# Optimization experiments

Hardware: AMD Instinct MI355X
Metric: run time of the kernel (lower is better)

Reference implementation:

```python
import jax, jax.numpy as jnp
import numpy as np

B, T, C, H = 8, 1024, 1024, 16
HD = C // H  # head dim = 64
NEG = -1e9


def setup_inputs() -> dict:
    key = jax.random.key(0)
    ks = jax.random.split(key, 10)
    total = B * T
    x = jax.random.normal(ks[0], (total, C), dtype=jnp.float32)
    # identity pack: each padded row is a contiguous chunk of tokens
    padpack_index = jnp.arange(total, dtype=jnp.int64).reshape(B, T)
    # sorted per-row sequence ids -> block-diagonal attention within each packed row
    padpack_batch = jnp.sort(jax.random.randint(ks[1], (B, T), 0, 4, dtype=jnp.int32), axis=-1)
    padpack_inverse_index = jnp.arange(total, dtype=jnp.int64)
    s = 1.0 / np.sqrt(C)
    Wq = jax.random.uniform(ks[2], (C, C), jnp.float32, -s, s)
    bq = jax.random.uniform(ks[3], (C,), jnp.float32, -s, s)
    Wk = jax.random.uniform(ks[4], (C, C), jnp.float32, -s, s)
    bk = jax.random.uniform(ks[5], (C,), jnp.float32, -s, s)
    Wv = jax.random.uniform(ks[6], (C, C), jnp.float32, -s, s)
    bv = jax.random.uniform(ks[7], (C,), jnp.float32, -s, s)
    Wp = jax.random.uniform(ks[8], (C, C), jnp.float32, -s, s)
    bp = jax.random.uniform(ks[9], (C,), jnp.float32, -s, s)
    return {"x": x, "padpack_index": padpack_index, "padpack_batch": padpack_batch,
            "padpack_inverse_index": padpack_inverse_index,
            "Wq": Wq, "bq": bq, "Wk": Wk, "bk": bk, "Wv": Wv, "bv": bv, "Wp": Wp, "bp": bp}


def reference(x, padpack_index, padpack_batch, padpack_inverse_index,
              Wq, bq, Wk, bk, Wv, bv, Wp, bp):
    # gather ragged tokens into padded [B, T, C]
    xp = x[padpack_index]
    # torch Linear: y = x @ W.T + b
    q = (xp @ Wq.T + bq).reshape(B, T, H, HD)
    k = (xp @ Wk.T + bk).reshape(B, T, H, HD)
    v = (xp @ Wv.T + bv).reshape(B, T, H, HD)
    scale = 1.0 / np.sqrt(HD).astype(np.float32)
    att = jnp.einsum('bihd,bjhd->bhij', q, k) * scale  # [B,H,T,T]
    # mask: token pairs from different packed sequences cannot attend
    mask = (padpack_batch[:, :, None] != padpack_batch[:, None, :])[:, None]  # [B,1,T,T]
    att = jnp.where(mask, NEG, att)
    att = jax.nn.softmax(att, axis=-1)
    y = jnp.einsum('bhij,bjhd->bihd', att, v).reshape(B, T, C)
    y = y @ Wp.T + bp
    # scatter back to ragged layout [total_tokens, C]
    return y.reshape(B * T, C)[padpack_inverse_index]
```

## Files before the change

### kernel.cpp

```cpp
#include <hip/hip_runtime.h>


typedef __attribute__((ext_vector_type(8))) short short8;
typedef __attribute__((ext_vector_type(4))) float f32x4;

#define MFMA16(a, b, c) __builtin_amdgcn_mfma_f32_16x16x32_bf16((a), (b), (c), 0, 0, 0)

__device__ __forceinline__ ushort f2b(float f) {
  union { float f; unsigned u; } v; v.f = f;
  unsigned u = v.u;
  return (ushort)((u + 0x7fffu + ((u >> 16) & 1u)) >> 16);
}

__device__ __forceinline__ void gload16(const void* g, void* l) {
  __builtin_amdgcn_global_load_lds((const __attribute__((address_space(1))) unsigned int*)g,
                                   (__attribute__((address_space(3))) unsigned int*)l,
                                   16, 0, 0);
}

__device__ __forceinline__ void cvt4(const float* __restrict__ s, ushort* __restrict__ d) {
  const float4 v = *(const float4*)s;
  ushort4 r; r.x = f2b(v.x); r.y = f2b(v.y); r.z = f2b(v.z); r.w = f2b(v.w);
  *(ushort4*)d = r;
}

__global__ __launch_bounds__(256) void prep(const float* __restrict__ x,
    const float* __restrict__ wq, const float* __restrict__ wk,
    const float* __restrict__ wv, const float* __restrict__ wp,
    ushort* __restrict__ xb, ushort* __restrict__ wb) {
  const long long e0 = ((long long)blockIdx.x * 256 + threadIdx.x) * 4;
  const long long NX = 8388608ll;
  if (e0 < NX) {
    cvt4(x + e0, xb + e0);
  } else {
    const long long t = e0 - NX;
    const int sel = (int)(t >> 20);
    const float* w = sel == 0 ? wq : sel == 1 ? wk : sel == 2 ? wv : wp;
    cvt4(w + (t & 1048575), wb + t);
  }
}

__global__ void seg_bounds(const int* __restrict__ pb, int* __restrict__ bnd) {
  const int b = blockIdx.x, i = threadIdx.x;
  const int* p = pb + b * 1024;
  const int cur = p[i];
  const int prev = (i == 0) ? -1 : p[i - 1];
  for (int v = prev + 1; v <= cur; ++v) bnd[b * 8 + v] = i;
  if (i == 1023)
    for (int v = cur + 1; v <= 4; ++v) bnd[b * 8 + v] = 1024;
}

template <int BN, int WM, int WN, int MODE>
__global__ __launch_bounds__(512, 2) void gemm8(
    const ushort* __restrict__ A, const ushort* __restrict__ Bw,
    const float* __restrict__ bias0, const float* __restrict__ bias1,
    const float* __restrict__ bias2,
    ushort* __restrict__ O0, ushort* __restrict__ O1, ushort* __restrict__ O2,
    float* __restrict__ Of) {
  constexpr int BM = 256;
  constexpr int MREP = BM / (WM * 16);
  constexpr int NREP = BN / (WN * 16);
  constexpr int ACH = BM * 64;
  constexpr int BCH = BN * 64;
  constexpr int GLA = ACH / 8192;
  constexpr int GLB = BCH / 8192;
  constexpr int GL = GLA + GLB;
  constexpr int BUFB = 2 * (ACH + BCH);
  __shared__ __align__(16) char smem[2 * BUFB];

  const int tid = threadIdx.x, lane = tid & 63, wid = tid >> 6;
  const int wr = wid / WN, wc = wid % WN;
  const int lg = lane >> 4, lc = lane & 15;

  const int id = blockIdx.x;
  const int s = id >> 3;
  const int m0 = ((id & 7) * 4 + (s & 3)) << 8;
  const int n0 = (s >> 2) * BN;

  f32x4 acc[MREP][NREP] = {};

  const int sr0 = tid >> 2;
  const int sc0 = (tid & 3) ^ ((sr0 >> 1) & 3);

#define STAGE_PAIR(p, kh, kt) { \
    char* ad = smem + (p) * BUFB + (kh) * ACH; \
    char* bd = smem + (p) * BUFB + 2 * ACH + (kh) * BCH; \
    const int kcol = (kt) * 64 + (kh) * 32; \
    gload16(A + (size_t)(m0 + sr0) * 1024 + kcol + sc0 * 8, ad + tid * 16); \
    if constexpr (GLA == 2) \
      gload16(A + (size_t)(m0 + 128 + sr0) * 1024 + kcol + sc0 * 8, ad + (tid + 512) * 16); \
    gload16(Bw + (size_t)(n0 + sr0) * 1024 + kcol + sc0 * 8, bd + tid * 16); \
    if constexpr (GLB == 2) \
      gload16(Bw + (size_t)(n0 + 128 + sr0) * 1024 + kcol + sc0 * 8, bd + (tid + 512) * 16); \
  }

#define PHASE_COMPUTE(p, kh) { \
    const char* ab = smem + (p) * BUFB + (kh) * ACH; \
    const char* bb = smem + (p) * BUFB + 2 * ACH + (kh) * BCH; \
    short8 af[MREP]; short8 bf[NREP]; \
    _Pragma("unroll") \
    for (int f = 0; f < MREP; ++f) { \
      const int row = wr * (MREP * 16) + f * 16 + lc; \
      af[f] = *(const short8*)(ab + row * 64 + ((lg ^ ((row >> 1) & 3)) << 4)); \
    } \
    _Pragma("unroll") \
    for (int g = 0; g < NREP; ++g) { \
      const int row = wc * (NREP * 16) + g * 16 + lc; \
      bf[g] = *(const short8*)(bb + row * 64 + ((lg ^ ((row >> 1) & 3)) << 4)); \
    } \
    asm volatile("s_waitcnt lgkmcnt(0)" ::: "memory"); \
    __builtin_amdgcn_sched_barrier(0); \
    __builtin_amdgcn_s_setprio(1); \
    _Pragma("unroll") \
    for (int f = 0; f < MREP; ++f) \
      _Pragma("unroll") \
      for (int g = 0; g < NREP; ++g) \
        acc[f][g] = MFMA16(af[f], bf[g], acc[f][g]); \
    __builtin_amdgcn_s_setprio(0); \
  }

#define WAIT_VM_GL() { \
    if constexpr (GL == 4) asm volatile("s_waitcnt vmcnt(4)" ::: "memory"); \
    else asm volatile("s_waitcnt vmcnt(3)" ::: "memory"); }

  STAGE_PAIR(0, 0, 0)
  STAGE_PAIR(0, 1, 0)

#pragma unroll 2
  for (int i = 0; i < 30; ++i) {
    const int t = i >> 1, kh = i & 1, p = t & 1;
    WAIT_VM_GL()
    __builtin_amdgcn_s_barrier();
    __builtin_amdgcn_sched_barrier(0);
    STAGE_PAIR(p ^ 1, kh, t + 1)
    PHASE_COMPUTE(p, kh)
  }
  WAIT_VM_GL()
  __builtin_amdgcn_s_barrier();
  __builtin_amdgcn_sched_barrier(0);
  PHASE_COMPUTE(1, 0)
  asm volatile("s_waitcnt vmcnt(0)" ::: "memory");
  __builtin_amdgcn_s_barrier();
  __builtin_amdgcn_sched_barrier(0);
  PHASE_COMPUTE(1, 1)

  if constexpr (MODE == 0) {
    const int sel = n0 >> 10, nloc = n0 & 1023;
    const float* bias = sel == 0 ? bias0 : sel == 1 ? bias1 : bias2;
    float bval[NREP];
#pragma unroll
    for (int g = 0; g < NREP; ++g) bval[g] = bias[nloc + wc * (NREP * 16) + g * 16 + lc];
    if (sel < 2) {
      ushort* dst = sel ? O1 : O0;
#pragma unroll
      for (int f = 0; f < MREP; ++f)
#pragma unroll
        for (int j = 0; j < 4; ++j) {
          const size_t row = m0 + wr * (MREP * 16) + f * 16 + lg * 4 + j;
#pragma unroll
          for (int g = 0; g < NREP; ++g)
            dst[row * 1024 + nloc + wc * (NREP * 16) + g * 16 + lc] =
                f2b(acc[f][g][j] + bval[g]);
        }
    } else {
      ushort (*Ts)[264] = (ushort(*)[264])smem;
#pragma unroll
      for (int mh = 0; mh < 2; ++mh) {
        __syncthreads();
        if (wr == mh) {
#pragma unroll
          for (int f = 0; f < MREP; ++f)
#pragma unroll
            for (int g = 0; g < NREP; ++g)
#pragma unroll
              for (int j = 0; j < 4; ++j)
                Ts[f * 16 + lg * 4 + j][wc * (NREP * 16) + g * 16 + lc] =
                    f2b(acc[f][g][j] + bval[g]);
        }
        __syncthreads();
        const int c = tid >> 1, th = (tid & 1) * 64;
        const int gt = m0 + mh * 128;
        const int b = gt >> 10, t0 = (gt & 1023) + th;
        const int gc = nloc + c;
        ushort* dp = O2 + ((size_t)((b * 16 + (gc >> 6)) * 64 + (gc & 63))) * 1024 + t0;
#pragma unroll
        for (int gb = 0; gb < 8; ++gb) {
          short8 pk;
#pragma unroll
          for (int u = 0; u < 8; ++u) pk[u] = (short)Ts[th + gb * 8 + u][c];
          *(short8*)(dp + gb * 8) = pk;
        }
      }
    }
  } else {
    float bval[NREP];
#pragma unroll
    for (int g = 0; g < NREP; ++g) bval[g] = bias0[n0 + wc * (NREP * 16) + g * 16 + lc];
#pragma unroll
    for (int f = 0; f < MREP; ++f)
#pragma unroll
      for (int j = 0; j < 4; ++j) {
        const size_t row = m0 + wr * (MREP * 16) + f * 16 + lg * 4 + j;
#pragma unroll
        for (int g = 0; g < NREP; ++g)
          Of[row * 1024 + n0 + wc * (NREP * 16) + g * 16 + lc] = acc[f][g][j] + bval[g];
      }
  }
#undef STAGE_PAIR
#undef PHASE_COMPUTE
#undef WAIT_VM_GL
}

__global__ __launch_bounds__(256) void attn(const ushort* __restrict__ Q,
    const ushort* __restrict__ K, const ushort* __restrict__ Vt,
    const int* __restrict__ bnd, ushort* __restrict__ O) {
  __shared__ __align__(16) char kvbuf[2][16384];
  __shared__ __align__(16) ushort Plds[4][16][68];

  const int tid = threadIdx.x, lane = tid & 63, w = tid >> 6;
  const int lg = lane >> 4, lc = lane & 15;

  const int id = blockIdx.x;
  const int xcd = id & 7, slot = id >> 3;
  const int bh = xcd + 8 * (slot >> 4), qt = slot & 15;
  const int b = bh >> 4, h = bh & 15;
  const int q0 = qt * 64 + w * 16;

  const int* bd = bnd + b * 8;
  const int b1 = bd[1], b2 = bd[2], b3 = bd[3], b4 = bd[4];
#define SEGID(k) (((k) >= b1) + ((k) >= b2) + ((k) >= b3) + ((k) >= b4))

  const int qid = SEGID(q0 + lc);
  int klo_l = (qid > 0) ? b1 : 0;
  klo_l = (qid > 1) ? b2 : klo_l;
  klo_l = (qid > 2) ? b3 : klo_l;
  int khi_l = (qid > 0) ? b2 : b1;
  khi_l = (qid > 1) ? b3 : khi_l;
  khi_l = (qid > 2) ? b4 : khi_l;

  const int bq_lo = SEGID(qt * 64), bq_hi = SEGID(qt * 64 + 63);
  unsigned am = 0;
#pragma unroll
  for (int jt = 0; jt < 16; ++jt) {
    const int tlo = SEGID(jt * 64), thi = SEGID(jt * 64 + 63);
    if (thi >= bq_lo && tlo <= bq_hi) am |= (1u << jt);
  }

  const ushort* qp = Q + (size_t)(b * 1024 + q0 + lc) * 1024 + h * 64 + lg * 8;
  const short8 qf0 = *(const short8*)qp;
  const short8 qf1 = *(const short8*)(qp + 32);

  const int r0 = tid >> 3;
  const int c16 = (tid & 7) ^ (r0 & 7);
  const ushort* Kg0 = K + (size_t)(b * 1024 + r0) * 1024 + h * 64 + c16 * 8;
  const ushort* Kg1 = Kg0 + (size_t)32 * 1024;
  const ushort* Vg0 = Vt + (size_t)(bh * 64 + r0) * 1024 + c16 * 8;
  const ushort* Vg1 = Vg0 + (size_t)32 * 1024;

#define STAGE(bufp, j) { \
    gload16(Kg0 + (size_t)(j) * 1024, (bufp) + tid * 16); \
    gload16(Kg1 + (size_t)(j) * 1024, (bufp) + 4096 + tid * 16); \
    gload16(Vg0 + (j), (bufp) + 8192 + tid * 16); \
    gload16(Vg1 + (j), (bufp) + 12288 + tid * 16); }

#define SOFF(r, ch) ((r) * 128 + ((((ch) ^ ((r) & 7))) << 4))

  float mr = -1e30f, lr = 0.f;
  f32x4 o[4] = {};

  unsigned rem = am;
  int jc = __builtin_ctz(rem) * 64;
  rem &= rem - 1;
  STAGE(kvbuf[0], jc)
  __syncthreads();
  int cur = 0;

  for (;;) {
    int jn = -1;
    if (rem) {
      jn = __builtin_ctz(rem) * 64;
      rem &= rem - 1;
      STAGE(kvbuf[cur ^ 1], jn)
    }
    const char* bufK = kvbuf[cur];
    const char* bufV = kvbuf[cur] + 8192;

    short8 kf[8];
#pragma unroll
    for (int n = 0; n < 4; ++n) {
      const int rr = n * 16 + lc;
      kf[2 * n] = *(const short8*)(bufK + SOFF(rr, lg));
      kf[2 * n + 1] = *(const short8*)(bufK + SOFF(rr, lg + 4));
    }
    f32x4 s[4];
    __builtin_amdgcn_s_setprio(1);
#pragma unroll
    for (int n = 0; n < 4; ++n) {
      f32x4 z = {};
      z = MFMA16(kf[2 * n], qf0, z);
      s[n] = MFMA16(kf[2 * n + 1], qf1, z);
    }
    __builtin_amdgcn_s_setprio(0);

#pragma unroll
    for (int n = 0; n < 4; ++n) {
      const int kk = jc + n * 16 + lg * 4;
#pragma unroll
      for (int r = 0; r < 4; ++r) {
        const bool ok = (kk + r >= klo_l) && (kk + r < khi_l);
        s[n][r] = ok ? s[n][r] * 0.125f : -1e9f;
      }
    }

    float rm = fmaxf(fmaxf(fmaxf(s[0][0], s[0][1]), fmaxf(s[0][2], s[0][3])),
                     fmaxf(fmaxf(fmaxf(s[1][0], s[1][1]), fmaxf(s[1][2], s[1][3])),
                           fmaxf(fmaxf(fmaxf(s[2][0], s[2][1]), fmaxf(s[2][2], s[2][3])),
                                 fmaxf(fmaxf(s[3][0], s[3][1]), fmaxf(s[3][2], s[3][3])))));
    rm = fmaxf(rm, __shfl_xor(rm, 16));
    rm = fmaxf(rm, __shfl_xor(rm, 32));
    float mn = mr;
    if (!__all(rm <= mr + 8.f)) {
      mn = fmaxf(mr, rm);
      const float sf = __expf(mr - mn);
      mr = mn;
      lr *= sf;
      const float s0 = __shfl(sf, lg * 4 + 0);
      const float s1 = __shfl(sf, lg * 4 + 1);
      const float s2 = __shfl(sf, lg * 4 + 2);
      const float s3 = __shfl(sf, lg * 4 + 3);
#pragma unroll
      for (int n = 0; n < 4; ++n) {
        o[n][0] *= s0; o[n][1] *= s1; o[n][2] *= s2; o[n][3] *= s3;
      }
    }
    float rs = 0.f;
#pragma unroll
    for (int n = 0; n < 4; ++n)
#pragma unroll
      for (int r = 0; r < 4; ++r) {
        const float p = __expf(s[n][r] - mn);
        s[n][r] = p; rs += p;
      }
    rs += __shfl_xor(rs, 16);
    rs += __shfl_xor(rs, 32);
    lr += rs;

#pragma unroll
    for (int n = 0; n < 4; ++n) {
      ushort4 pk;
      pk.x = f2b(s[n][0]); pk.y = f2b(s[n][1]); pk.z = f2b(s[n][2]); pk.w = f2b(s[n][3]);
      *(ushort4*)&Plds[w][lc][n * 16 + lg * 4] = pk;
    }
    asm volatile("s_waitcnt lgkmcnt(0)" ::: "memory");
    __builtin_amdgcn_sched_barrier(0);
    const short8 p0 = *(const short8*)&Plds[w][lc][lg * 8];
    const short8 p1 = *(const short8*)&Plds[w][lc][32 + lg * 8];
    __builtin_amdgcn_sched_barrier(0);

    short8 vv[8];
#pragma unroll
    for (int n = 0; n < 4; ++n) {
      const int rr = n * 16 + lc;
      vv[2 * n] = *(const short8*)(bufV + SOFF(rr, lg));
      vv[2 * n + 1] = *(const short8*)(bufV + SOFF(rr, lg + 4));
    }
    __builtin_amdgcn_s_setprio(1);
#pragma unroll
    for (int n = 0; n < 4; ++n) {
      o[n] = MFMA16(p0, vv[2 * n], o[n]);
      o[n] = MFMA16(p1, vv[2 * n + 1], o[n]);
    }
    __builtin_amdgcn_s_setprio(0);

    if (jn < 0) break;
    __syncthreads();
    cur ^= 1;
    jc = jn;
  }

  const float linv = 1.f / lr;
  const float i0 = __shfl(linv, lg * 4 + 0);
  const float i1 = __shfl(linv, lg * 4 + 1);
  const float i2 = __shfl(linv, lg * 4 + 2);
  const float i3 = __shfl(linv, lg * 4 + 3);
#pragma unroll
  for (int n = 0; n < 4; ++n) {
    const size_t base = (size_t)(b * 1024 + q0) * 1024 + h * 64 + n * 16 + lc;
    O[base + 0 * 1024 + (size_t)lg * 4096] = f2b(o[n][0] * i0);
    O[base + 1 * 1024 + (size_t)lg * 4096] = f2b(o[n][1] * i1);
    O[base + 2 * 1024 + (size_t)lg * 4096] = f2b(o[n][2] * i2);
    O[base + 3 * 1024 + (size_t)lg * 4096] = f2b(o[n][3] * i3);
  }
#undef STAGE
#undef SOFF
#undef SEGID
}

extern "C" void kernel_launch(void* const* d_in, const int* in_sizes, int n_in,
                              void* d_out, int out_size, void* d_ws, size_t ws_size,
                              hipStream_t stream) {
  const float* x  = (const float*)d_in[0];
  const int*  pb  = (const int*)d_in[2];
  const float* Wq = (const float*)d_in[4]; const float* bq = (const float*)d_in[5];
  const float* Wk = (const float*)d_in[6]; const float* bk = (const float*)d_in[7];
  const float* Wv = (const float*)d_in[8]; const float* bv = (const float*)d_in[9];
  const float* Wp = (const float*)d_in[10]; const float* bp = (const float*)d_in[11];
  float* out = (float*)d_out;
  char* ws = (char*)d_ws;

  ushort* xb = (ushort*)ws;
  ushort* wb = (ushort*)(ws + (16u << 20));
  ushort* Qb = (ushort*)(ws + (24u << 20));
  ushort* Kb = (ushort*)(ws + (40u << 20));
  ushort* Vt = (ushort*)(ws + (56u << 20));
  int*    bnd = (int*)(ws + (72u << 20));
  ushort* Ob = xb;

  prep<<<12288, 256, 0, stream>>>(x, Wq, Wk, Wv, Wp, xb, wb);
  seg_bounds<<<8, 1024, 0, stream>>>(pb, bnd);
  gemm8<256, 2, 4, 0><<<384, 512, 0, stream>>>(xb, wb, bq, bk, bv, Qb, Kb, Vt, nullptr);
  attn<<<2048, 256, 0, stream>>>(Qb, Kb, Vt, bnd, Ob);
  gemm8<128, 4, 2, 1><<<256, 512, 0, stream>>>(Ob, wb + (3 << 20), bp,
                                               nullptr, nullptr, nullptr, nullptr, nullptr, out);
}
```

Measured before the change: 156.1 us.

## Triple-buffer GEMM staging and shrink QKV tile to 256x128

The GEMM kernel now uses three LDS buffers, so loads for k-tile t+2 are issued while tile t is computed, replacing the previous double buffering with deeper prefetch. The QKV projection drops from 256x256 tiles to 256x128 tiles, doubling its grid to 768 blocks for better CU fill; both GEMMs now share one fixed tile shape. The cost is more LDS per block (144KB), which may restrict occupancy to one block per CU despite launch_bounds(512,2), plus more redundant A-tile loads in the QKV GEMM.

```diff
diff --git a/kernel.cpp b/kernel.cpp
--- a/kernel.cpp
+++ b/kernel.cpp
@@ -50,141 +50,149 @@
     for (int v = cur + 1; v <= 4; ++v) bnd[b * 8 + v] = 1024;
 }
 
-template <int BN, int WM, int WN, int MODE>
+template <int MODE>
 __global__ __launch_bounds__(512, 2) void gemm8(
     const ushort* __restrict__ A, const ushort* __restrict__ Bw,
     const float* __restrict__ bias0, const float* __restrict__ bias1,
     const float* __restrict__ bias2,
     ushort* __restrict__ O0, ushort* __restrict__ O1, ushort* __restrict__ O2,
     float* __restrict__ Of) {
-  constexpr int BM = 256;
-  constexpr int MREP = BM / (WM * 16);
-  constexpr int NREP = BN / (WN * 16);
-  constexpr int ACH = BM * 64;
-  constexpr int BCH = BN * 64;
-  constexpr int GLA = ACH / 8192;
-  constexpr int GLB = BCH / 8192;
-  constexpr int GL = GLA + GLB;
+  constexpr int ACH = 256 * 64;
+  constexpr int BCH = 128 * 64;
   constexpr int BUFB = 2 * (ACH + BCH);
-  __shared__ __align__(16) char smem[2 * BUFB];
+  __shared__ __align__(16) char smem[3 * BUFB];
 
   const int tid = threadIdx.x, lane = tid & 63, wid = tid >> 6;
-  const int wr = wid / WN, wc = wid % WN;
+  const int wr = wid >> 1, wc = wid & 1;
   const int lg = lane >> 4, lc = lane & 15;
 
   const int id = blockIdx.x;
   const int s = id >> 3;
   const int m0 = ((id & 7) * 4 + (s & 3)) << 8;
-  const int n0 = (s >> 2) * BN;
-
-  f32x4 acc[MREP][NREP] = {};
+  const int n0 = (s >> 2) << 7;
+
+  f32x4 acc[4][4] = {};
 
   const int sr0 = tid >> 2;
   const int sc0 = (tid & 3) ^ ((sr0 >> 1) & 3);
 
-#define STAGE_PAIR(p, kh, kt) { \
-    char* ad = smem + (p) * BUFB + (kh) * ACH; \
-    char* bd = smem + (p) * BUFB + 2 * ACH + (kh) * BCH; \
+#define STAGE(dst_, kh, kt) { \
+    char* ad = (dst_) + (kh) * ACH; \
+    char* bd = (dst_) + 2 * ACH + (kh) * BCH; \
     const int kcol = (kt) * 64 + (kh) * 32; \
     gload16(A + (size_t)(m0 + sr0) * 1024 + kcol + sc0 * 8, ad + tid * 16); \
-    if constexpr (GLA == 2) \
-      gload16(A + (size_t)(m0 + 128 + sr0) * 1024 + kcol + sc0 * 8, ad + (tid + 512) * 16); \
+    gload16(A + (size_t)(m0 + 128 + sr0) * 1024 + kcol + sc0 * 8, ad + (tid + 512) * 16); \
     gload16(Bw + (size_t)(n0 + sr0) * 1024 + kcol + sc0 * 8, bd + tid * 16); \
-    if constexpr (GLB == 2) \
-      gload16(Bw + (size_t)(n0 + 128 + sr0) * 1024 + kcol + sc0 * 8, bd + (tid + 512) * 16); \
-  }
-
-#define PHASE_COMPUTE(p, kh) { \
-    const char* ab = smem + (p) * BUFB + (kh) * ACH; \
-    const char* bb = smem + (p) * BUFB + 2 * ACH + (kh) * BCH; \
-    short8 af[MREP]; short8 bf[NREP]; \
+  }
+
+#define PHASE_COMPUTE(src_, kh) { \
+    const char* ab = (src_) + (kh) * ACH; \
+    const char* bb = (src_) + 2 * ACH + (kh) * BCH; \
+    short8 af[4]; short8 bf[4]; \
     _Pragma("unroll") \
-    for (int f = 0; f < MREP; ++f) { \
-      const int row = wr * (MREP * 16) + f * 16 + lc; \
+    for (int f = 0; f < 4; ++f) { \
+      const int row = wr * 64 + f * 16 + lc; \
       af[f] = *(const short8*)(ab + row * 64 + ((lg ^ ((row >> 1) & 3)) << 4)); \
     } \
     _Pragma("unroll") \
-    for (int g = 0; g < NREP; ++g) { \
-      const int row = wc * (NREP * 16) + g * 16 + lc; \
+    for (int g = 0; g < 4; ++g) { \
+      const int row = wc * 64 + g * 16 + lc; \
       bf[g] = *(const short8*)(bb + row * 64 + ((lg ^ ((row >> 1) & 3)) << 4)); \
     } \
     asm volatile("s_waitcnt lgkmcnt(0)" ::: "memory"); \
     __builtin_amdgcn_sched_barrier(0); \
     __builtin_amdgcn_s_setprio(1); \
     _Pragma("unroll") \
-    for (int f = 0; f < MREP; ++f) \
+    for (int f = 0; f < 4; ++f) \
       _Pragma("unroll") \
-      for (int g = 0; g < NREP; ++g) \
+      for (int g = 0; g < 4; ++g) \
         acc[f][g] = MFMA16(af[f], bf[g], acc[f][g]); \
     __builtin_amdgcn_s_setprio(0); \
   }
 
-#define WAIT_VM_GL() { \
-    if constexpr (GL == 4) asm volatile("s_waitcnt vmcnt(4)" ::: "memory"); \
-    else asm volatile("s_waitcnt vmcnt(3)" ::: "memory"); }
-
-  STAGE_PAIR(0, 0, 0)
-  STAGE_PAIR(0, 1, 0)
-
-#pragma unroll 2
-  for (int i = 0; i < 30; ++i) {
-    const int t = i >> 1, kh = i & 1, p = t & 1;
-    WAIT_VM_GL()
+#define WAITVM(n) { asm volatile("s_waitcnt vmcnt(" #n ")" ::: "memory"); }
+
+  char* b0 = smem;
+  char* b1 = smem + BUFB;
+  char* b2 = smem + 2 * BUFB;
+
+  STAGE(b0, 0, 0)
+  STAGE(b0, 1, 0)
+  STAGE(b1, 0, 1)
+  STAGE(b1, 1, 1)
+
+  for (int t = 0; t < 14; ++t) {
+    WAITVM(9)
     __builtin_amdgcn_s_barrier();
     __builtin_amdgcn_sched_barrier(0);
-    STAGE_PAIR(p ^ 1, kh, t + 1)
-    PHASE_COMPUTE(p, kh)
-  }
-  WAIT_VM_GL()
+    STAGE(b2, 0, t + 2)
+    PHASE_COMPUTE(b0, 0)
+    WAITVM(9)
+    __builtin_amdgcn_s_barrier();
+    __builtin_amdgcn_sched_barrier(0);
+    STAGE(b2, 1, t + 2)
+    PHASE_COMPUTE(b0, 1)
+    char* tmp = b0; b0 = b1; b1 = b2; b2 = tmp;
+  }
+  WAITVM(9)
   __builtin_amdgcn_s_barrier();
   __builtin_amdgcn_sched_barrier(0);
-  PHASE_COMPUTE(1, 0)
-  asm volatile("s_waitcnt vmcnt(0)" ::: "memory");
+  PHASE_COMPUTE(b0, 0)
+  WAITVM(6)
   __builtin_amdgcn_s_barrier();
   __builtin_amdgcn_sched_barrier(0);
-  PHASE_COMPUTE(1, 1)
+  PHASE_COMPUTE(b0, 1)
+  WAITVM(3)
+  __builtin_amdgcn_s_barrier();
+  __builtin_amdgcn_sched_barrier(0);
+  PHASE_COMPUTE(b1, 0)
+  WAITVM(0)
+  __builtin_amdgcn_s_barrier();
+  __builtin_amdgcn_sched_barrier(0);
+  PHASE_COMPUTE(b1, 1)
 
   if constexpr (MODE == 0) {
     const int sel = n0 >> 10, nloc = n0 & 1023;
     const float* bias = sel == 0 ? bias0 : sel == 1 ? bias1 : bias2;
-    float bval[NREP];
-#pragma unroll
-    for (int g = 0; g < NREP; ++g) bval[g] = bias[nloc + wc * (NREP * 16) + g * 16 + lc];
+    float bval[4];
+#pragma unroll
+    for (int g = 0; g < 4; ++g) bval[g] = bias[nloc + wc * 64 + g * 16 + lc];
     if (sel < 2) {
       ushort* dst = sel ? O1 : O0;
 #pragma unroll
-      for (int f = 0; f < MREP; ++f)
+      for (int f = 0; f < 4; ++f)
 #pragma unroll
         for (int j = 0; j < 4; ++j) {
-          const size_t row = m0 + wr * (MREP * 16) + f * 16 + lg * 4 + j;
-#pragma unroll
-          for (int g = 0; g < NREP; ++g)
-            dst[row * 1024 + nloc + wc * (NREP * 16) + g * 16 + lc] =
-                f2b(acc[f][g][j] + bval[g]);
+          const size_t row = m0 + wr * 64 + f * 16 + lg * 4 + j;
+#pragma unroll
+          for (int g = 0; g < 4; ++g)
+            dst[row * 1024 + nloc + wc * 64 + g * 16 + lc] = f2b(acc[f][g][j] + bval[g]);
         }
     } else {
-      ushort (*Ts)[264] = (ushort(*)[264])smem;
+      ushort (*Ts)[136] = (ushort(*)[136])smem;
 #pragma unroll
       for (int mh = 0; mh < 2; ++mh) {
         __syncthreads();
-        if (wr == mh) {
-#pragma unroll
-          for (int f = 0; f < MREP; ++f)
-#pragma unroll
-            for (int g = 0; g < NREP; ++g)
+        if ((wr >> 1) == mh) {
+#pragma unroll
+          for (int f = 0; f < 4; ++f)
+#pragma unroll
+            for (int g = 0; g < 4; ++g)
 #pragma unroll
               for (int j = 0; j < 4; ++j)
-                Ts[f * 16 + lg * 4 + j][wc * (NREP * 16) + g * 16 + lc] =
+                Ts[(wr & 1) * 64 + f * 16 + lg * 4 + j][wc * 64 + g * 16 + lc] =
                     f2b(acc[f][g][j] + bval[g]);
         }
         __syncthreads();
-        const int c = tid >> 1, th = (tid & 1) * 64;
+        const int c = tid >> 2;
+        const int th = (tid & 3) * 32;
         const int gt = m0 + mh * 128;
-        const int b = gt >> 10, t0 = (gt & 1023) + th;
+        const int b = gt >> 10;
+        const int t0 = (gt & 1023) + th;
         const int gc = nloc + c;
         ushort* dp = O2 + ((size_t)((b * 16 + (gc >> 6)) * 64 + (gc & 63))) * 1024 + t0;
 #pragma unroll
-        for (int gb = 0; gb < 8; ++gb) {
+        for (int gb = 0; gb < 4; ++gb) {
           short8 pk;
 #pragma unroll
           for (int u = 0; u < 8; ++u) pk[u] = (short)Ts[th + gb * 8 + u][c];
@@ -193,22 +201,22 @@
       }
     }
   } else {
-    float bval[NREP];
-#pragma unroll
-    for (int g = 0; g < NREP; ++g) bval[g] = bias0[n0 + wc * (NREP * 16) + g * 16 + lc];
-#pragma unroll
-    for (int f = 0; f < MREP; ++f)
+    float bval[4];
+#pragma unroll
+    for (int g = 0; g < 4; ++g) bval[g] = bias0[n0 + wc * 64 + g * 16 + lc];
+#pragma unroll
+    for (int f = 0; f < 4; ++f)
 #pragma unroll
       for (int j = 0; j < 4; ++j) {
-        const size_t row = m0 + wr * (MREP * 16) + f * 16 + lg * 4 + j;
-#pragma unroll
-        for (int g = 0; g < NREP; ++g)
-          Of[row * 1024 + n0 + wc * (NREP * 16) + g * 16 + lc] = acc[f][g][j] + bval[g];
+        const size_t row = m0 + wr * 64 + f * 16 + lg * 4 + j;
+#pragma unroll
+        for (int g = 0; g < 4; ++g)
+          Of[row * 1024 + n0 + wc * 64 + g * 16 + lc] = acc[f][g][j] + bval[g];
       }
   }
-#undef STAGE_PAIR
+#undef STAGE
 #undef PHASE_COMPUTE
-#undef WAIT_VM_GL
+#undef WAITVM
 }
 
 __global__ __launch_bounds__(256) void attn(const ushort* __restrict__ Q,
@@ -418,8 +426,8 @@
 
   prep<<<12288, 256, 0, stream>>>(x, Wq, Wk, Wv, Wp, xb, wb);
   seg_bounds<<<8, 1024, 0, stream>>>(pb, bnd);
-  gemm8<256, 2, 4, 0><<<384, 512, 0, stream>>>(xb, wb, bq, bk, bv, Qb, Kb, Vt, nullptr);
+  gemm8<0><<<768, 512, 0, stream>>>(xb, wb, bq, bk, bv, Qb, Kb, Vt, nullptr);
   attn<<<2048, 256, 0, stream>>>(Qb, Kb, Vt, bnd, Ob);
-  gemm8<128, 4, 2, 1><<<256, 512, 0, stream>>>(Ob, wb + (3 << 20), bp,
-                                               nullptr, nullptr, nullptr, nullptr, nullptr, out);
-}
+  gemm8<1><<<256, 512, 0, stream>>>(Ob, wb + (3 << 20), bp,
+                                    nullptr, nullptr, nullptr, nullptr, nullptr, out);
+}
```

Measured after the change: 155.2 us. About the same (-0.6%).
